# Kernel optimization log

Measured on AMD Instinct MI355X. Metric: run time of the kernel, lower is better.

The kernel has to match this reference:

```python
import jax, jax.numpy as jnp
import numpy as np

B, S, V, E, H, C = 16384, 64, 25, 64, 64, 3

def setup_inputs() -> dict:
    key = jax.random.key(0)
    ks = jax.random.split(key, 5)
    return {
        "messages": jax.random.normal(ks[0], (B, S, V), dtype=jnp.float32),
        "embedding": jax.random.normal(ks[1], (V, E), dtype=jnp.float32) * 0.1,
        "W_ih": jax.random.normal(ks[2], (4 * H, E), dtype=jnp.float32) * 0.1,
        "W_hh": jax.random.normal(ks[3], (4 * H, H), dtype=jnp.float32) * 0.1,
        "b_ih": jnp.zeros((4 * H,), dtype=jnp.float32),
        "b_hh": jnp.zeros((4 * H,), dtype=jnp.float32).at[H:2 * H].set(1.0),
        "fc_w": jax.random.normal(ks[4], (C, H), dtype=jnp.float32) * 0.1,
        "fc_b": jnp.zeros((C,), dtype=jnp.float32),
    }

def _lstm_forward(emb_t, W_ih, W_hh, b_ih, b_hh):
    # emb_t: [S, B, E] time-major. PyTorch LSTMCell gate order: i, f, g, o.
    batch = emb_t.shape[1]
    h0 = jnp.zeros((batch, W_hh.shape[1]), dtype=emb_t.dtype)
    c0 = jnp.zeros_like(h0)
    # Precompute input projections for all steps in one big GEMM.
    x_proj = jnp.einsum('sbe,ge->sbg', emb_t, W_ih) + b_ih + b_hh  # [S, B, 4H]

    def step(carry, xp):
        h, c = carry
        gates = xp + h @ W_hh.T  # [B, 4H]
        i, f, g, o = jnp.split(gates, 4, axis=-1)
        i = jax.nn.sigmoid(i)
        f = jax.nn.sigmoid(f)
        g = jnp.tanh(g)
        o = jax.nn.sigmoid(o)
        c_new = f * c + i * g
        h_new = o * jnp.tanh(c_new)
        return (h_new, c_new), None

    (h_final, _), _ = jax.lax.scan(step, (h0, c0), x_proj)
    return h_final

def reference(messages, embedding, W_ih, W_hh, b_ih, b_hh, fc_w, fc_b):
    emb = jnp.einsum('bsv,ve->bse', messages, embedding)  # [B, S, E]
    emb_t = jnp.transpose(emb, (1, 0, 2))                 # [S, B, E]
    h = _lstm_forward(emb_t, W_ih, W_hh, b_ih, b_hh)      # [B, H]
    fc_out = h @ fc_w.T + fc_b                            # [B, C]
    return jnp.squeeze(fc_out)
```

## Files before the change

kernel.cpp:

```cpp
#include <hip/hip_runtime.h>
#include <math.h>


using bf16x8 = __attribute__((ext_vector_type(8))) short;
using f32x4  = __attribute__((ext_vector_type(4))) float;

union U16B { uint4 u; bf16x8 v; };

#define KE  1.4426950408889634f
#define K2E 2.8853900817779268f

__device__ __forceinline__ unsigned short f2bf(float x) {
    unsigned int u = __float_as_uint(x);
    u += 0x7FFFu + ((u >> 16) & 1u);
    return (unsigned short)(u >> 16);
}
__device__ __forceinline__ float bf2f(unsigned short h) {
    return __uint_as_float(((unsigned int)h) << 16);
}

__global__ void prep_kernel(const float* __restrict__ emb,
                            const float* __restrict__ Wih,
                            const float* __restrict__ Whh,
                            const float* __restrict__ bih,
                            const float* __restrict__ bhh,
                            unsigned short* __restrict__ wfrag) {
    const int b = blockIdx.x, tid = threadIdx.x;
    const int ch = b >> 4, gt = b & 15;
    const int lane = tid >> 3, j = tid & 7;
    const int kloc = (lane >> 4) * 8 + j;
    const int gunit = 16 * gt + (lane & 15);
    float v = 0.f;
    if (ch == 0) {
        if (kloc < 25) {
            const float* ep = emb + kloc * 64;
            const float* wp = Wih + gunit * 64;
            float s = 0.f;
            #pragma unroll
            for (int e = 0; e < 64; ++e) s = fmaf(ep[e], wp[e], s);
            v = s;
        } else if (kloc == 25) {
            v = bih[gunit] + bhh[gunit];
        }
    } else {
        v = Whh[gunit * 64 + (ch - 1) * 32 + kloc];
    }
    const int gate = gunit >> 6;
    const float s = (gate == 2) ? K2E : -KE;
    wfrag[((ch * 16 + gt) * 64 + lane) * 8 + j] = f2bf(s * v);
}

#define CVTPK(D, A, B_)                                                      \
    asm("v_cvt_pk_bf16_f32 %0, %1, %2" : "=v"(D) : "v"(A), "v"(B_));

#define LOADMSG(DST, SS)                                                     \
    {                                                                        \
        const float* p_ = mrow + (SS) * 25 + kq;                             \
        if (kq < 24) {                                                       \
            float t0_ = p_[0], t1_ = p_[1], t2_ = p_[2], t3_ = p_[3];        \
            float t4_ = p_[4], t5_ = p_[5], t6_ = p_[6], t7_ = p_[7];        \
            CVTPK(DST.u.x, t0_, t1_) CVTPK(DST.u.y, t2_, t3_)                \
            CVTPK(DST.u.z, t4_, t5_) CVTPK(DST.u.w, t6_, t7_)                \
        } else {                                                             \
            float t0_ = p_[0], one_ = 1.0f;                                  \
            CVTPK(DST.u.x, t0_, one_)                                        \
            DST.u.y = 0u; DST.u.z = 0u; DST.u.w = 0u;                        \
        }                                                                    \
    }

#define STEP(S, CURB, NXTB, MC, MN)                                          \
    {                                                                        \
        if ((S) < 63) LOADMSG(MN, (S) + 1)                                   \
        bf16x8 bh[2];                                                        \
        _Pragma("unroll") for (int ch = 0; ch < 2; ++ch) {                   \
            int off_ = (l16 * 128 + ch * 64 + lq * 16) ^ swz;                \
            bh[ch] = *(const bf16x8*)((CURB) + off_);                        \
        }                                                                    \
        f32x4 acc[4];                                                        \
        _Pragma("unroll") for (int i = 0; i < 4; ++i)                        \
            acc[i] = (f32x4){0.f, 0.f, 0.f, 0.f};                           \
        _Pragma("unroll") for (int i = 0; i < 4; ++i)                        \
            acc[i] = __builtin_amdgcn_mfma_f32_16x16x32_bf16(                \
                w[0][i], MC.v, acc[i], 0, 0, 0);                             \
        _Pragma("unroll") for (int ch = 0; ch < 2; ++ch)                     \
            _Pragma("unroll") for (int i = 0; i < 4; ++i)                    \
                acc[i] = __builtin_amdgcn_mfma_f32_16x16x32_bf16(            \
                    w[1 + ch][i], bh[ch], acc[i], 0, 0, 0);                  \
        float hn[4];                                                         \
        _Pragma("unroll") for (int q = 0; q < 4; ++q) {                      \
            float ai = acc[0][q], af = acc[1][q];                            \
            float ag = acc[2][q], ao = acc[3][q];                            \
            float ti = __builtin_amdgcn_exp2f(ai);                           \
            float tf = __builtin_amdgcn_exp2f(af);                           \
            float to = __builtin_amdgcn_exp2f(ao);                           \
            float tg = __builtin_amdgcn_exp2f(-fabsf(ag));                   \
            float ig = (1.f - tg) *                                          \
                __builtin_amdgcn_rcpf((1.f + ti) * (1.f + tg));              \
            ig = copysignf(ig, ag);                                          \
            float fg = __builtin_amdgcn_rcpf(1.f + tf);                      \
            float cn = fmaf(fg, c[q], ig);                                   \
            c[q] = cn;                                                       \
            float tc = __builtin_amdgcn_exp2f(-fabsf(K2E * cn));             \
            float ot = (1.f - tc) *                                          \
                __builtin_amdgcn_rcpf((1.f + to) * (1.f + tc));              \
            hn[q] = copysignf(ot, cn);                                       \
        }                                                                    \
        unsigned r01_, r23_;                                                 \
        CVTPK(r01_, hn[0], hn[1]) CVTPK(r23_, hn[2], hn[3])                  \
        *(uint2*)((NXTB) + offw) = make_uint2(r01_, r23_);                   \
        __syncthreads();                                                     \
    }

__global__ __launch_bounds__(256, 4) void lstm_mfma(
    const float* __restrict__ msgs,
    const unsigned short* __restrict__ wfrag,
    const float* __restrict__ fcw,
    const float* __restrict__ fcb,
    float* __restrict__ out)
{
    __shared__ __align__(16) char lds[4096];

    const int tid  = threadIdx.x;
    const int lane = tid & 63;
    const int cg   = __builtin_amdgcn_readfirstlane(tid >> 6);
    const int l16  = lane & 15;
    const int lq   = lane >> 4;
    const int row0 = blockIdx.x * 16;
    const int kq   = lq * 8;

    bf16x8 w[3][4];
    #pragma unroll
    for (int ch = 0; ch < 3; ++ch)
        #pragma unroll
        for (int i = 0; i < 4; ++i)
            w[ch][i] = *(const bf16x8*)(wfrag + ((ch * 16 + 4 * i + cg) * 64 + lane) * 8);

    for (int idx = tid; idx < 512; idx += 256) ((unsigned int*)lds)[idx] = 0u;

    float c[4] = {0.f, 0.f, 0.f, 0.f};

    const float* mrow = msgs + (long)(row0 + l16) * 1600;
    const int swz  = (l16 & 7) << 4;
    const int offw = (l16 * 128 + cg * 32 + lq * 8) ^ swz;

    U16B m0, m1;
    LOADMSG(m0, 0)
    __syncthreads();

    char* b0 = (char*)lds;
    char* b1 = b0 + 2048;
    for (int s2 = 0; s2 < 64; s2 += 2) {
        STEP(s2,     b0, b1, m0, m1)
        STEP(s2 + 1, b1, b0, m1, m0)
    }

    if (tid < 64) {
        const int r = tid >> 2, cls = tid & 3;
        if (cls < 3) {
            float a = fcb[cls];
            const int sw = (r & 7) << 4;
            #pragma unroll
            for (int u = 0; u < 64; ++u) {
                int off = (r * 128 + u * 2) ^ sw;
                float hv = bf2f(*(const unsigned short*)(b0 + off));
                a = fmaf(hv, fcw[cls * 64 + u], a);
            }
            out[(row0 + r) * 3 + cls] = a;
        }
    }
}

extern "C" void kernel_launch(void* const* d_in, const int* in_sizes, int n_in,
                              void* d_out, int out_size, void* d_ws, size_t ws_size,
                              hipStream_t stream) {
    const float* msgs = (const float*)d_in[0];
    const float* emb  = (const float*)d_in[1];
    const float* Wih  = (const float*)d_in[2];
    const float* Whh  = (const float*)d_in[3];
    const float* bih  = (const float*)d_in[4];
    const float* bhh  = (const float*)d_in[5];
    const float* fcw  = (const float*)d_in[6];
    const float* fcb  = (const float*)d_in[7];
    float* out = (float*)d_out;

    unsigned short* wfrag = (unsigned short*)d_ws;

    prep_kernel<<<48, 512, 0, stream>>>(emb, Wih, Whh, bih, bhh, wfrag);
    lstm_mfma<<<16384 / 16, 256, 0, stream>>>(msgs, wfrag, fcw, fcb, out);
}
```

Before: 112.3 us.

## Run each 16-row LSTM tile in a single wavefront with register-resident hidden state

Each block now uses one 64-lane wavefront instead of four. The wavefront computes all 256 gate units per step, with 48 MFMAs per step instead of 12 per wave. The hidden state stays in registers because the W_hh K-ordering is permuted in prep so the MFMA output layout matches the B-operand layout. This removes the per-step LDS round trip and __syncthreads barrier, and the final FC becomes a cross-lane shuffle reduction. In exchange, per-wave register pressure rises sharply (48 weight fragments plus 16 accumulators), and there are fewer waves per CU to hide MFMA and transcendental latency.

```diff
diff --git a/kernel.cpp b/kernel.cpp
--- a/kernel.cpp
+++ b/kernel.cpp
@@ -43,7 +43,10 @@
             v = bih[gunit] + bhh[gunit];
         }
     } else {
-        v = Whh[gunit * 64 + (ch - 1) * 32 + kloc];
+        const int jj = kloc & 7, lqk = kloc >> 3;
+        const int unit = (ch - 1) * 32 +
+            ((jj < 4) ? (4 * lqk + jj) : (16 + 4 * lqk + (jj - 4)));
+        v = Whh[gunit * 64 + unit];
     }
     const int gate = gunit >> 6;
     const float s = (gate == 2) ? K2E : -KE;
@@ -68,105 +71,118 @@
         }                                                                    \
     }
 
-#define STEP(S, CURB, NXTB, MC, MN)                                          \
+#define STEP(S, MC, MN, BHC, BHN)                                            \
     {                                                                        \
         if ((S) < 63) LOADMSG(MN, (S) + 1)                                   \
-        bf16x8 bh[2];                                                        \
-        _Pragma("unroll") for (int ch = 0; ch < 2; ++ch) {                   \
-            int off_ = (l16 * 128 + ch * 64 + lq * 16) ^ swz;                \
-            bh[ch] = *(const bf16x8*)((CURB) + off_);                        \
+        f32x4 acc[4][4];                                                     \
+        _Pragma("unroll") for (int u = 0; u < 4; ++u)                        \
+            _Pragma("unroll") for (int i = 0; i < 4; ++i)                    \
+                acc[u][i] = (f32x4){0.f, 0.f, 0.f, 0.f};                     \
+        _Pragma("unroll") for (int u = 0; u < 4; ++u)                        \
+            _Pragma("unroll") for (int i = 0; i < 4; ++i)                    \
+                acc[u][i] = __builtin_amdgcn_mfma_f32_16x16x32_bf16(         \
+                    w[4 * i + u], MC.v, acc[u][i], 0, 0, 0);                 \
+        _Pragma("unroll") for (int u = 0; u < 4; ++u)                        \
+            _Pragma("unroll") for (int i = 0; i < 4; ++i)                    \
+                acc[u][i] = __builtin_amdgcn_mfma_f32_16x16x32_bf16(         \
+                    w[16 + 4 * i + u], BHC[0].v, acc[u][i], 0, 0, 0);        \
+        _Pragma("unroll") for (int u = 0; u < 4; ++u)                        \
+            _Pragma("unroll") for (int i = 0; i < 4; ++i)                    \
+                acc[u][i] = __builtin_amdgcn_mfma_f32_16x16x32_bf16(         \
+                    w[32 + 4 * i + u], BHC[1].v, acc[u][i], 0, 0, 0);        \
+        _Pragma("unroll") for (int u = 0; u < 4; ++u) {                      \
+            float hn[4];                                                     \
+            _Pragma("unroll") for (int q = 0; q < 4; ++q) {                  \
+                float ai = acc[u][0][q], af = acc[u][1][q];                  \
+                float ag = acc[u][2][q], ao = acc[u][3][q];                  \
+                float ti = __builtin_amdgcn_exp2f(ai);                       \
+                float tf = __builtin_amdgcn_exp2f(af);                       \
+                float to = __builtin_amdgcn_exp2f(ao);                       \
+                float tg = __builtin_amdgcn_exp2f(-fabsf(ag));               \
+                float ig = (1.f - tg) *                                      \
+                    __builtin_amdgcn_rcpf((1.f + ti) * (1.f + tg));          \
+                ig = copysignf(ig, ag);                                      \
+                float fg = __builtin_amdgcn_rcpf(1.f + tf);                  \
+                float cn = fmaf(fg, c[u][q], ig);                            \
+                c[u][q] = cn;                                                \
+                float tc = __builtin_amdgcn_exp2f(-fabsf(K2E * cn));         \
+                float ot = (1.f - tc) *                                      \
+                    __builtin_amdgcn_rcpf((1.f + to) * (1.f + tc));          \
+                hn[q] = copysignf(ot, cn);                                   \
+            }                                                                \
+            unsigned pa_, pb_;                                               \
+            CVTPK(pa_, hn[0], hn[1]) CVTPK(pb_, hn[2], hn[3])                \
+            if (u == 0) { BHN[0].u.x = pa_; BHN[0].u.y = pb_; }              \
+            if (u == 1) { BHN[0].u.z = pa_; BHN[0].u.w = pb_; }              \
+            if (u == 2) { BHN[1].u.x = pa_; BHN[1].u.y = pb_; }              \
+            if (u == 3) { BHN[1].u.z = pa_; BHN[1].u.w = pb_; }              \
         }                                                                    \
-        f32x4 acc[4];                                                        \
-        _Pragma("unroll") for (int i = 0; i < 4; ++i)                        \
-            acc[i] = (f32x4){0.f, 0.f, 0.f, 0.f};                           \
-        _Pragma("unroll") for (int i = 0; i < 4; ++i)                        \
-            acc[i] = __builtin_amdgcn_mfma_f32_16x16x32_bf16(                \
-                w[0][i], MC.v, acc[i], 0, 0, 0);                             \
-        _Pragma("unroll") for (int ch = 0; ch < 2; ++ch)                     \
-            _Pragma("unroll") for (int i = 0; i < 4; ++i)                    \
-                acc[i] = __builtin_amdgcn_mfma_f32_16x16x32_bf16(            \
-                    w[1 + ch][i], bh[ch], acc[i], 0, 0, 0);                  \
-        float hn[4];                                                         \
-        _Pragma("unroll") for (int q = 0; q < 4; ++q) {                      \
-            float ai = acc[0][q], af = acc[1][q];                            \
-            float ag = acc[2][q], ao = acc[3][q];                            \
-            float ti = __builtin_amdgcn_exp2f(ai);                           \
-            float tf = __builtin_amdgcn_exp2f(af);                           \
-            float to = __builtin_amdgcn_exp2f(ao);                           \
-            float tg = __builtin_amdgcn_exp2f(-fabsf(ag));                   \
-            float ig = (1.f - tg) *                                          \
-                __builtin_amdgcn_rcpf((1.f + ti) * (1.f + tg));              \
-            ig = copysignf(ig, ag);                                          \
-            float fg = __builtin_amdgcn_rcpf(1.f + tf);                      \
-            float cn = fmaf(fg, c[q], ig);                                   \
-            c[q] = cn;                                                       \
-            float tc = __builtin_amdgcn_exp2f(-fabsf(K2E * cn));             \
-            float ot = (1.f - tc) *                                          \
-                __builtin_amdgcn_rcpf((1.f + to) * (1.f + tc));              \
-            hn[q] = copysignf(ot, cn);                                       \
-        }                                                                    \
-        unsigned r01_, r23_;                                                 \
-        CVTPK(r01_, hn[0], hn[1]) CVTPK(r23_, hn[2], hn[3])                  \
-        *(uint2*)((NXTB) + offw) = make_uint2(r01_, r23_);                   \
-        __syncthreads();                                                     \
-    }
-
-__global__ __launch_bounds__(256, 4) void lstm_mfma(
+    }
+
+__global__ __launch_bounds__(64, 1) void lstm_mfma(
     const float* __restrict__ msgs,
     const unsigned short* __restrict__ wfrag,
     const float* __restrict__ fcw,
     const float* __restrict__ fcb,
     float* __restrict__ out)
 {
-    __shared__ __align__(16) char lds[4096];
-
-    const int tid  = threadIdx.x;
-    const int lane = tid & 63;
-    const int cg   = __builtin_amdgcn_readfirstlane(tid >> 6);
+    const int lane = threadIdx.x;
     const int l16  = lane & 15;
     const int lq   = lane >> 4;
     const int row0 = blockIdx.x * 16;
     const int kq   = lq * 8;
 
-    bf16x8 w[3][4];
-    #pragma unroll
-    for (int ch = 0; ch < 3; ++ch)
+    bf16x8 w[48];
+    #pragma unroll
+    for (int t = 0; t < 48; ++t)
+        w[t] = *(const bf16x8*)(wfrag + (t * 64 + lane) * 8);
+
+    float c[4][4];
+    #pragma unroll
+    for (int u = 0; u < 4; ++u)
         #pragma unroll
-        for (int i = 0; i < 4; ++i)
-            w[ch][i] = *(const bf16x8*)(wfrag + ((ch * 16 + 4 * i + cg) * 64 + lane) * 8);
-
-    for (int idx = tid; idx < 512; idx += 256) ((unsigned int*)lds)[idx] = 0u;
-
-    float c[4] = {0.f, 0.f, 0.f, 0.f};
+        for (int q = 0; q < 4; ++q) c[u][q] = 0.f;
+
+    U16B bhA[2], bhB[2];
+    bhA[0].u = make_uint4(0u, 0u, 0u, 0u);
+    bhA[1].u = make_uint4(0u, 0u, 0u, 0u);
 
     const float* mrow = msgs + (long)(row0 + l16) * 1600;
-    const int swz  = (l16 & 7) << 4;
-    const int offw = (l16 * 128 + cg * 32 + lq * 8) ^ swz;
 
     U16B m0, m1;
     LOADMSG(m0, 0)
-    __syncthreads();
-
-    char* b0 = (char*)lds;
-    char* b1 = b0 + 2048;
+
     for (int s2 = 0; s2 < 64; s2 += 2) {
-        STEP(s2,     b0, b1, m0, m1)
-        STEP(s2 + 1, b1, b0, m1, m0)
-    }
-
-    if (tid < 64) {
-        const int r = tid >> 2, cls = tid & 3;
-        if (cls < 3) {
-            float a = fcb[cls];
-            const int sw = (r & 7) << 4;
-            #pragma unroll
-            for (int u = 0; u < 64; ++u) {
-                int off = (r * 128 + u * 2) ^ sw;
-                float hv = bf2f(*(const unsigned short*)(b0 + off));
-                a = fmaf(hv, fcw[cls * 64 + u], a);
-            }
-            out[(row0 + r) * 3 + cls] = a;
+        STEP(s2,     m0, m1, bhA, bhB)
+        STEP(s2 + 1, m1, m0, bhB, bhA)
+    }
+
+    float a0 = 0.f, a1 = 0.f, a2 = 0.f;
+    #pragma unroll
+    for (int g = 0; g < 4; ++g) {
+        #pragma unroll
+        for (int q = 0; q < 4; ++q) {
+            unsigned uw = (g & 1) ? ((q >> 1) ? bhA[g >> 1].u.w : bhA[g >> 1].u.z)
+                                  : ((q >> 1) ? bhA[g >> 1].u.y : bhA[g >> 1].u.x);
+            float hv = (q & 1) ? __uint_as_float(uw & 0xFFFF0000u)
+                               : __uint_as_float(uw << 16);
+            int n = 16 * g + 4 * lq + q;
+            a0 = fmaf(hv, fcw[n], a0);
+            a1 = fmaf(hv, fcw[64 + n], a1);
+            a2 = fmaf(hv, fcw[128 + n], a2);
         }
+    }
+    #pragma unroll
+    for (int mask = 16; mask <= 32; mask <<= 1) {
+        a0 += __shfl_xor(a0, mask, 64);
+        a1 += __shfl_xor(a1, mask, 64);
+        a2 += __shfl_xor(a2, mask, 64);
+    }
+    if (lq == 0) {
+        float* op = out + (long)(row0 + l16) * 3;
+        op[0] = a0 + fcb[0];
+        op[1] = a1 + fcb[1];
+        op[2] = a2 + fcb[2];
     }
 }
 
@@ -186,5 +202,5 @@
     unsigned short* wfrag = (unsigned short*)d_ws;
 
     prep_kernel<<<48, 512, 0, stream>>>(emb, Wih, Whh, bih, bhh, wfrag);
-    lstm_mfma<<<16384 / 16, 256, 0, stream>>>(msgs, wfrag, fcw, fcb, out);
-}
+    lstm_mfma<<<16384 / 16, 64, 0, stream>>>(msgs, wfrag, fcw, fcb, out);
+}
```

Result: slower. 118.4 us (+5.4%).
